# Kernel optimization log

Hardware: AMD Instinct MI355X
Metric: run time of the kernel (lower is better)

## Reference

```python
import jax, jax.numpy as jnp
import numpy as np

D_MODEL = 1024
N_HEADS = 16
HEAD_DIM = 64
BATCH = 4
SEQ = 2048


def setup_inputs() -> dict:
    key = jax.random.key(0)
    ks = jax.random.split(key, 5)
    scale = 1.0 / np.sqrt(D_MODEL)
    return {
        "x": jax.random.normal(ks[0], (BATCH, SEQ, D_MODEL), dtype=jnp.float32),
        "Wq": jax.random.normal(ks[1], (D_MODEL, N_HEADS * HEAD_DIM), dtype=jnp.float32) * scale,
        "Wk": jax.random.normal(ks[2], (D_MODEL, N_HEADS * HEAD_DIM), dtype=jnp.float32) * scale,
        "Wv": jax.random.normal(ks[3], (D_MODEL, N_HEADS * HEAD_DIM), dtype=jnp.float32) * scale,
        "Wo": jax.random.normal(ks[4], (N_HEADS * HEAD_DIM, D_MODEL), dtype=jnp.float32) * scale,
        "bo": jnp.zeros((D_MODEL,), dtype=jnp.float32),
    }


def reference(x, Wq, Wk, Wv, Wo, bo):
    B, S, _ = x.shape
    H, Dh = N_HEADS, HEAD_DIM
    # projections -> [B, H, S, Dh]
    q = (x @ Wq).reshape(B, S, H, Dh).transpose(0, 2, 1, 3)
    k = (x @ Wk).reshape(B, S, H, Dh).transpose(0, 2, 1, 3)
    v = (x @ Wv).reshape(B, S, H, Dh).transpose(0, 2, 1, 3)
    score = jnp.einsum("bhsd,bhtd->bhst", q, k) / jnp.sqrt(jnp.float32(Dh))
    causal = jnp.triu(jnp.ones((S, S), dtype=bool), k=1)
    score = jnp.where(causal, -jnp.inf, score)
    attn_probs = jax.nn.softmax(score, axis=-1)
    # dropout is identity in eval mode
    attn = jnp.einsum("bhst,bhtd->bhsd", attn_probs, v)
    out = attn.transpose(0, 2, 1, 3).reshape(B, S, H * Dh)
    out = out @ Wo + bo
    return (out, attn_probs)
```

## Files before the change

kernel.cpp:

```cpp
#include <hip/hip_runtime.h>
#include <hip/hip_bf16.h>

typedef __attribute__((ext_vector_type(8))) short bf16x8;
typedef __attribute__((ext_vector_type(4))) float f32x4;
typedef unsigned short ushort_t;

#define AS1 __attribute__((address_space(1)))
#define AS3 __attribute__((address_space(3)))

__device__ __forceinline__ void gload_lds16(const void* g, void* l) {
    __builtin_amdgcn_global_load_lds((const AS1 void*)g, (AS3 void*)l, 16, 0, 0);
}

__device__ __forceinline__ ushort_t f2b(float f) {
    unsigned u = __builtin_bit_cast(unsigned, f);
    unsigned r = (u + 0x7FFFu + ((u >> 16) & 1u)) >> 16;
    return (ushort_t)r;
}

__device__ __forceinline__ float b2f(short s) {
    unsigned v = ((unsigned)(ushort_t)s) << 16;
    return __builtin_bit_cast(float, v);
}

__global__ __launch_bounds__(256) void convert_x_kernel(const float* __restrict__ in,
                                                        ushort_t* __restrict__ out, int n4) {
    int i = blockIdx.x * blockDim.x + threadIdx.x;
    if (i < n4) {
        float4 f = ((const float4*)in)[i];
        ushort4 u;
        u.x = f2b(f.x); u.y = f2b(f.y); u.z = f2b(f.z); u.w = f2b(f.w);
        ((ushort4*)out)[i] = u;
    }
}

__global__ __launch_bounds__(256) void transpose_w_kernel(const float* __restrict__ W,
                                                          ushort_t* __restrict__ WT) {
    __shared__ float t[32][33];
    int n0 = blockIdx.x * 32, k0 = blockIdx.y * 32;
    int tx = threadIdx.x, ty = threadIdx.y;
    for (int i = 0; i < 4; ++i)
        t[ty + i * 8][tx] = W[(size_t)(k0 + ty + i * 8) * 1024 + n0 + tx];
    __syncthreads();
    for (int i = 0; i < 4; ++i)
        WT[(size_t)(n0 + ty + i * 8) * 1024 + k0 + tx] = f2b(t[tx][ty + i * 8]);
}

template <int N, int OUT_BF16>
__global__ __launch_bounds__(256) void gemm_kernel(const ushort_t* __restrict__ A,
                                                   const ushort_t* __restrict__ BT,
                                                   ushort_t* __restrict__ Cb,
                                                   float* __restrict__ Cf,
                                                   const float* __restrict__ bias) {
    const int K = 1024;
    __shared__ ushort_t As[2 * 128 * 32];
    __shared__ ushort_t Bs[2 * 128 * 32];
    int tid = threadIdx.x;
    int wid = tid >> 6, lane = tid & 63;
    int g = lane >> 4, lr = lane & 15;
    int m0 = blockIdx.x * 128, n0 = blockIdx.y * 128;
    int wm = wid >> 1, wn = wid & 1;

    f32x4 acc[4][4] = {};

    int c0 = wid * 2;
    int lrow = lane >> 2;
    int lcol = ((lane & 3) ^ ((lane >> 3) & 3)) * 8;
    const ushort_t* Ag0 = A  + (size_t)(m0 + c0 * 16 + lrow) * K + lcol;
    const ushort_t* Ag1 = A  + (size_t)(m0 + c0 * 16 + 16 + lrow) * K + lcol;
    const ushort_t* Bg0 = BT + (size_t)(n0 + c0 * 16 + lrow) * K + lcol;
    const ushort_t* Bg1 = BT + (size_t)(n0 + c0 * 16 + 16 + lrow) * K + lcol;

    int swzA = ((lr >> 1) & 3) << 4;

    auto stage = [&](int bufi, int kt) {
        char* a0 = (char*)As + bufi * 8192 + c0 * 1024;
        char* b0 = (char*)Bs + bufi * 8192 + c0 * 1024;
        gload_lds16(Ag0 + kt * 32, a0);
        gload_lds16(Ag1 + kt * 32, a0 + 1024);
        gload_lds16(Bg0 + kt * 32, b0);
        gload_lds16(Bg1 + kt * 32, b0 + 1024);
    };

    stage(0, 0);
    __syncthreads();
    int buf = 0;
    for (int kt = 0; kt < K / 32; ++kt) {
        if (kt + 1 < K / 32) stage(buf ^ 1, kt + 1);
        const char* ab = (const char*)As + buf * 8192;
        const char* bb = (const char*)Bs + buf * 8192;
        bf16x8 af[4], bfr[4];
#pragma unroll
        for (int m = 0; m < 4; ++m) {
            int row = wm * 64 + m * 16 + lr;
            af[m] = *(const bf16x8*)(ab + row * 64 + ((g * 16) ^ swzA));
        }
#pragma unroll
        for (int n = 0; n < 4; ++n) {
            int row = wn * 64 + n * 16 + lr;
            bfr[n] = *(const bf16x8*)(bb + row * 64 + ((g * 16) ^ swzA));
        }
#pragma unroll
        for (int m = 0; m < 4; ++m)
#pragma unroll
            for (int n = 0; n < 4; ++n)
                acc[m][n] = __builtin_amdgcn_mfma_f32_16x16x32_bf16(af[m], bfr[n], acc[m][n], 0, 0, 0);
        __syncthreads();
        buf ^= 1;
    }

#pragma unroll
    for (int m = 0; m < 4; ++m)
#pragma unroll
        for (int n = 0; n < 4; ++n) {
            int row0 = m0 + wm * 64 + m * 16 + g * 4;
            int col  = n0 + wn * 64 + n * 16 + lr;
#pragma unroll
            for (int r = 0; r < 4; ++r) {
                float v = acc[m][n][r];
                if (OUT_BF16)
                    Cb[(size_t)(row0 + r) * N + col] = f2b(v);
                else
                    Cf[(size_t)(row0 + r) * N + col] = v + bias[col];
            }
        }
}

__global__ __launch_bounds__(256) void vt_kernel(const ushort_t* __restrict__ Cqkv,
                                                 ushort_t* __restrict__ Vt) {
    int b = blockIdx.z, h = blockIdx.y, st = blockIdx.x;
    __shared__ ushort_t t[64][72];
    const ushort_t* src = Cqkv + (size_t)b * 2048 * 3072 + 2048 + (size_t)h * 64;
    int tid = threadIdx.x;
#pragma unroll
    for (int i = 0; i < 2; ++i) {
        int c = tid + i * 256;
        int sl = c >> 3, dc = (c & 7) * 8;
        *(bf16x8*)&t[sl][dc] = *(const bf16x8*)(src + (size_t)(st * 64 + sl) * 3072 + dc);
    }
    __syncthreads();
#pragma unroll
    for (int i = 0; i < 2; ++i) {
        int c = tid + i * 256;
        int d = c >> 3, sc = (c & 7) * 8;
        bf16x8 v;
#pragma unroll
        for (int j = 0; j < 8; ++j) v[j] = (short)t[sc + j][d];
        *(bf16x8*)(Vt + ((size_t)(b * 16 + h) * 64 + d) * 2048 + st * 64 + sc) = v;
    }
}

__global__ __launch_bounds__(256) void attn_kernel(const ushort_t* __restrict__ Cqkv,
                                                   const ushort_t* __restrict__ Vtg,
                                                   float* __restrict__ Pout,
                                                   ushort_t* __restrict__ Oout) {
    const int S = 2048, DQ = 3072;
    const float C1 = 0.18033688f;
    const float C2 = 5.77078016f;

    int z = (int)blockIdx.x + 32 * (int)blockIdx.y + 512 * (int)blockIdx.z;
    int h = (z >> 5) & 15, b = z >> 9;
    int qt = ((z & 31) + 13 * ((z >> 8) & 7)) & 31;
    int q0 = qt * 64;

    int tid = threadIdx.x, wid = tid >> 6, lane = tid & 63;
    int g = lane >> 4, lr = lane & 15;

    __shared__ ushort_t Ks[2][4096];
    __shared__ ushort_t Vs[2][4096];
    __shared__ ushort_t Pb[4096];
    char* PbB = (char*)Pb;

    const ushort_t* Qb = Cqkv + (size_t)b * S * DQ + (size_t)h * 64;
    const ushort_t* Kb = Cqkv + (size_t)b * S * DQ + 1024 + (size_t)h * 64;
    const ushort_t* Vb = Vtg + (size_t)((b * 16 + h) * 64) * 2048;
    float* Pbase = Pout + (((size_t)(b * 16 + h)) * S + q0) * S;

    int srow = lane >> 3;
    int scol = ((lane & 7) ^ (lane >> 3)) * 8;

    auto stageK = [&](int bufi, int tt) {
        char* dst = (char*)&Ks[bufi][0] + wid * 1024;
        gload_lds16(Kb + (size_t)(tt * 64 + wid * 8 + srow) * DQ + scol, dst);
        gload_lds16(Kb + (size_t)(tt * 64 + 32 + wid * 8 + srow) * DQ + scol, dst + 4096);
    };
    auto stageV = [&](int bufi, int tt) {
        char* dst = (char*)&Vs[bufi][0] + wid * 1024;
        gload_lds16(Vb + (size_t)(wid * 8 + srow) * 2048 + tt * 64 + scol, dst);
        gload_lds16(Vb + (size_t)(32 + wid * 8 + srow) * 2048 + tt * 64 + scol, dst + 4096);
    };

    bf16x8 qf[2];
    {
        const ushort_t* qp = Qb + (size_t)(q0 + wid * 16 + lr) * DQ + g * 8;
        qf[0] = *(const bf16x8*)qp;
        qf[1] = *(const bf16x8*)(qp + 32);
    }
    int qlg = wid * 16 + g * 4;

    float psum[4] = {0.f, 0.f, 0.f, 0.f};
    stageK(0, 0);
    __syncthreads();
    int buf = 0;
    for (int tt = 0; tt <= qt; ++tt) {
        if (tt < qt) stageK(buf ^ 1, tt + 1);
        const char* ksb = (const char*)&Ks[buf][0];
#pragma unroll
        for (int nb = 0; nb < 4; ++nb) {
            int row = nb * 16 + lr;
            int x = (row & 7) << 4;
            f32x4 s = {};
            s = __builtin_amdgcn_mfma_f32_16x16x32_bf16(qf[0], *(const bf16x8*)(ksb + row * 128 + ((g * 16) ^ x)), s, 0, 0, 0);
            s = __builtin_amdgcn_mfma_f32_16x16x32_bf16(qf[1], *(const bf16x8*)(ksb + row * 128 + ((64 + g * 16) ^ x)), s, 0, 0, 0);
            if (tt == qt) {
#pragma unroll
                for (int r = 0; r < 4; ++r)
                    if (row <= qlg + r) psum[r] += exp2f(fmaf(s[r], C1, -C2));
            } else {
#pragma unroll
                for (int r = 0; r < 4; ++r) psum[r] += exp2f(fmaf(s[r], C1, -C2));
            }
        }
        __syncthreads();
        buf ^= 1;
    }
    float lnl2[4];
#pragma unroll
    for (int r = 0; r < 4; ++r) {
        float v = psum[r];
        v += __shfl_xor(v, 1); v += __shfl_xor(v, 2);
        v += __shfl_xor(v, 4); v += __shfl_xor(v, 8);
        lnl2[r] = __log2f(v) + C2;
    }

    f32x4 Oacc[4] = {};
    stageK(buf, 0);
    stageV(buf, 0);
    __syncthreads();
    for (int tt = 0; tt <= qt; ++tt) {
        if (tt < qt) { stageK(buf ^ 1, tt + 1); stageV(buf ^ 1, tt + 1); }
        const char* ksb = (const char*)&Ks[buf][0];
        const char* vsb = (const char*)&Vs[buf][0];
#pragma unroll
        for (int nb = 0; nb < 4; ++nb) {
            int row = nb * 16 + lr;
            int x = (row & 7) << 4;
            f32x4 s = {};
            s = __builtin_amdgcn_mfma_f32_16x16x32_bf16(qf[0], *(const bf16x8*)(ksb + row * 128 + ((g * 16) ^ x)), s, 0, 0, 0);
            s = __builtin_amdgcn_mfma_f32_16x16x32_bf16(qf[1], *(const bf16x8*)(ksb + row * 128 + ((64 + g * 16) ^ x)), s, 0, 0, 0);
#pragma unroll
            for (int r = 0; r < 4; ++r) {
                float p = exp2f(fmaf(s[r], C1, -lnl2[r]));
                if (tt == qt && (row > qlg + r)) p = 0.f;
                int prow = qlg + r;
                *(ushort_t*)(PbB + ((prow * 128 + row * 2) ^ ((prow & 7) << 4))) = f2b(p);
            }
        }
        __builtin_amdgcn_wave_barrier();
#pragma unroll
        for (int kc = 0; kc < 2; ++kc) {
            int prow = wid * 16 + lr;
            bf16x8 pf = *(const bf16x8*)(PbB + ((prow * 128 + kc * 64 + g * 16) ^ ((prow & 7) << 4)));
#pragma unroll
            for (int nb = 0; nb < 4; ++nb) {
                int vrow = nb * 16 + lr;
                bf16x8 vf = *(const bf16x8*)(vsb + vrow * 128 + ((kc * 64 + g * 16) ^ ((vrow & 7) << 4)));
                Oacc[nb] = __builtin_amdgcn_mfma_f32_16x16x32_bf16(pf, vf, Oacc[nb], 0, 0, 0);
            }
        }
        {
            int row = wid * 16 + (lane >> 2);
            int c0 = (lane & 3) * 16;
            int x = (row & 7) << 4;
            bf16x8 p0 = *(const bf16x8*)(PbB + ((row * 128 + c0 * 2) ^ x));
            bf16x8 p1 = *(const bf16x8*)(PbB + ((row * 128 + c0 * 2 + 16) ^ x));
            float* dst = Pbase + (size_t)row * S + tt * 64 + c0;
            float4 w;
            w.x = b2f(p0[0]); w.y = b2f(p0[1]); w.z = b2f(p0[2]); w.w = b2f(p0[3]); ((float4*)dst)[0] = w;
            w.x = b2f(p0[4]); w.y = b2f(p0[5]); w.z = b2f(p0[6]); w.w = b2f(p0[7]); ((float4*)dst)[1] = w;
            w.x = b2f(p1[0]); w.y = b2f(p1[1]); w.z = b2f(p1[2]); w.w = b2f(p1[3]); ((float4*)dst)[2] = w;
            w.x = b2f(p1[4]); w.y = b2f(p1[5]); w.z = b2f(p1[6]); w.w = b2f(p1[7]); ((float4*)dst)[3] = w;
        }
        __syncthreads();
        buf ^= 1;
    }

    {
        int vsr = tid >> 2, vsc = (tid & 3) * 16;
        float4 zf = {0.f, 0.f, 0.f, 0.f};
        for (int tt = qt + 1; tt < 32; ++tt) {
            float* dst = Pbase + (size_t)vsr * S + tt * 64 + vsc;
#pragma unroll
            for (int j = 0; j < 4; ++j) ((float4*)dst)[j] = zf;
        }
    }

#pragma unroll
    for (int nb = 0; nb < 4; ++nb)
#pragma unroll
        for (int r = 0; r < 4; ++r) {
            int q = q0 + qlg + r;
            Oout[((size_t)b * S + q) * 1024 + h * 64 + nb * 16 + lr] = f2b(Oacc[nb][r]);
        }
}

extern "C" void kernel_launch(void* const* d_in, const int* in_sizes, int n_in,
                              void* d_out, int out_size, void* d_ws, size_t ws_size,
                              hipStream_t stream) {
    const float* x  = (const float*)d_in[0];
    const float* Wq = (const float*)d_in[1];
    const float* Wk = (const float*)d_in[2];
    const float* Wv = (const float*)d_in[3];
    const float* Wo = (const float*)d_in[4];
    const float* bo = (const float*)d_in[5];

    float* out  = (float*)d_out;
    float* Pout = out + (size_t)8388608;

    char* ws = (char*)d_ws;
    ushort_t* xb    = (ushort_t*)(ws);
    ushort_t* wqkv  = (ushort_t*)(ws + (16u << 20));
    ushort_t* wob   = (ushort_t*)(ws + (22u << 20));
    ushort_t* Cqkv  = (ushort_t*)(ws + (24u << 20));
    ushort_t* Vtw   = (ushort_t*)(ws + (72u << 20));
    ushort_t* attnb = (ushort_t*)(ws + (104u << 20));

    convert_x_kernel<<<8192, 256, 0, stream>>>(x, xb, 2097152);
    transpose_w_kernel<<<dim3(32, 32), dim3(32, 8), 0, stream>>>(Wq, wqkv);
    transpose_w_kernel<<<dim3(32, 32), dim3(32, 8), 0, stream>>>(Wk, wqkv + 1024 * 1024);
    transpose_w_kernel<<<dim3(32, 32), dim3(32, 8), 0, stream>>>(Wv, wqkv + 2 * 1024 * 1024);
    transpose_w_kernel<<<dim3(32, 32), dim3(32, 8), 0, stream>>>(Wo, wob);

    gemm_kernel<3072, 1><<<dim3(64, 24), 256, 0, stream>>>(xb, wqkv, Cqkv, nullptr, nullptr);

    vt_kernel<<<dim3(32, 16, 4), 256, 0, stream>>>(Cqkv, Vtw);

    attn_kernel<<<dim3(32, 16, 4), 256, 0, stream>>>(Cqkv, Vtw, Pout, attnb);

    gemm_kernel<1024, 0><<<dim3(64, 8), 256, 0, stream>>>(attnb, wob, nullptr, out, bo);
}
```

Baseline: 556.3 us.

## Transpose score MFMA so each lane owns a query row and stores P directly

The Q·K MFMA operands are swapped, so each lane holds four consecutive key scores for a single query row. This lets the probability tile go straight from registers to global memory as fp32 float4 stores, removing the staging through shared memory as bf16 and the read-back. The row-sum reduction becomes two cross-group shuffles instead of four. The bf16 copy for P·V is packed with v_cvt_pk_bf16_f32 into a per-wave LDS slice. The end-of-iteration __syncthreads is replaced by a vmcnt(4) wait plus s_barrier, so the P stores can stay in flight while the next tiles land; this relies on exact counting of outstanding memory ops.

```diff
diff --git a/kernel.cpp b/kernel.cpp
--- a/kernel.cpp
+++ b/kernel.cpp
@@ -4,6 +4,7 @@
 typedef __attribute__((ext_vector_type(8))) short bf16x8;
 typedef __attribute__((ext_vector_type(4))) float f32x4;
 typedef unsigned short ushort_t;
+typedef unsigned int uint_t;
 
 #define AS1 __attribute__((address_space(1)))
 #define AS3 __attribute__((address_space(3)))
@@ -16,11 +17,6 @@
     unsigned u = __builtin_bit_cast(unsigned, f);
     unsigned r = (u + 0x7FFFu + ((u >> 16) & 1u)) >> 16;
     return (ushort_t)r;
-}
-
-__device__ __forceinline__ float b2f(short s) {
-    unsigned v = ((unsigned)(ushort_t)s) << 16;
-    return __builtin_bit_cast(float, v);
 }
 
 __global__ __launch_bounds__(256) void convert_x_kernel(const float* __restrict__ in,
@@ -168,8 +164,8 @@
 
     __shared__ ushort_t Ks[2][4096];
     __shared__ ushort_t Vs[2][4096];
-    __shared__ ushort_t Pb[4096];
-    char* PbB = (char*)Pb;
+    __shared__ ushort_t Pl[4096];
+    char* PlB = (char*)Pl + wid * 2048;
 
     const ushort_t* Qb = Cqkv + (size_t)b * S * DQ + (size_t)h * 64;
     const ushort_t* Kb = Cqkv + (size_t)b * S * DQ + 1024 + (size_t)h * 64;
@@ -177,7 +173,7 @@
     float* Pbase = Pout + (((size_t)(b * 16 + h)) * S + q0) * S;
 
     int srow = lane >> 3;
-    int scol = ((lane & 7) ^ (lane >> 3)) * 8;
+    int scol = ((lane & 7) ^ srow) * 8;
 
     auto stageK = [&](int bufi, int tt) {
         char* dst = (char*)&Ks[bufi][0] + wid * 1024;
@@ -196,9 +192,9 @@
         qf[0] = *(const bf16x8*)qp;
         qf[1] = *(const bf16x8*)(qp + 32);
     }
-    int qlg = wid * 16 + g * 4;
-
-    float psum[4] = {0.f, 0.f, 0.f, 0.f};
+    int qloc = wid * 16 + lr;
+
+    float psum = 0.f;
     stageK(0, 0);
     __syncthreads();
     int buf = 0;
@@ -210,28 +206,23 @@
             int row = nb * 16 + lr;
             int x = (row & 7) << 4;
             f32x4 s = {};
-            s = __builtin_amdgcn_mfma_f32_16x16x32_bf16(qf[0], *(const bf16x8*)(ksb + row * 128 + ((g * 16) ^ x)), s, 0, 0, 0);
-            s = __builtin_amdgcn_mfma_f32_16x16x32_bf16(qf[1], *(const bf16x8*)(ksb + row * 128 + ((64 + g * 16) ^ x)), s, 0, 0, 0);
+            s = __builtin_amdgcn_mfma_f32_16x16x32_bf16(*(const bf16x8*)(ksb + row * 128 + ((g * 16) ^ x)), qf[0], s, 0, 0, 0);
+            s = __builtin_amdgcn_mfma_f32_16x16x32_bf16(*(const bf16x8*)(ksb + row * 128 + ((64 + g * 16) ^ x)), qf[1], s, 0, 0, 0);
             if (tt == qt) {
 #pragma unroll
                 for (int r = 0; r < 4; ++r)
-                    if (row <= qlg + r) psum[r] += exp2f(fmaf(s[r], C1, -C2));
+                    if (nb * 16 + g * 4 + r <= qloc) psum += exp2f(fmaf(s[r], C1, -C2));
             } else {
 #pragma unroll
-                for (int r = 0; r < 4; ++r) psum[r] += exp2f(fmaf(s[r], C1, -C2));
+                for (int r = 0; r < 4; ++r) psum += exp2f(fmaf(s[r], C1, -C2));
             }
         }
         __syncthreads();
         buf ^= 1;
     }
-    float lnl2[4];
-#pragma unroll
-    for (int r = 0; r < 4; ++r) {
-        float v = psum[r];
-        v += __shfl_xor(v, 1); v += __shfl_xor(v, 2);
-        v += __shfl_xor(v, 4); v += __shfl_xor(v, 8);
-        lnl2[r] = __log2f(v) + C2;
-    }
+    psum += __shfl_xor(psum, 16);
+    psum += __shfl_xor(psum, 32);
+    float lnl2 = __log2f(psum) + C2;
 
     f32x4 Oacc[4] = {};
     stageK(buf, 0);
@@ -241,26 +232,36 @@
         if (tt < qt) { stageK(buf ^ 1, tt + 1); stageV(buf ^ 1, tt + 1); }
         const char* ksb = (const char*)&Ks[buf][0];
         const char* vsb = (const char*)&Vs[buf][0];
+        f32x4 p[4];
 #pragma unroll
         for (int nb = 0; nb < 4; ++nb) {
             int row = nb * 16 + lr;
             int x = (row & 7) << 4;
             f32x4 s = {};
-            s = __builtin_amdgcn_mfma_f32_16x16x32_bf16(qf[0], *(const bf16x8*)(ksb + row * 128 + ((g * 16) ^ x)), s, 0, 0, 0);
-            s = __builtin_amdgcn_mfma_f32_16x16x32_bf16(qf[1], *(const bf16x8*)(ksb + row * 128 + ((64 + g * 16) ^ x)), s, 0, 0, 0);
+            s = __builtin_amdgcn_mfma_f32_16x16x32_bf16(*(const bf16x8*)(ksb + row * 128 + ((g * 16) ^ x)), qf[0], s, 0, 0, 0);
+            s = __builtin_amdgcn_mfma_f32_16x16x32_bf16(*(const bf16x8*)(ksb + row * 128 + ((64 + g * 16) ^ x)), qf[1], s, 0, 0, 0);
 #pragma unroll
             for (int r = 0; r < 4; ++r) {
-                float p = exp2f(fmaf(s[r], C1, -lnl2[r]));
-                if (tt == qt && (row > qlg + r)) p = 0.f;
-                int prow = qlg + r;
-                *(ushort_t*)(PbB + ((prow * 128 + row * 2) ^ ((prow & 7) << 4))) = f2b(p);
+                float v = exp2f(fmaf(s[r], C1, -lnl2));
+                if (tt == qt && (nb * 16 + g * 4 + r > qloc)) v = 0.f;
+                p[nb][r] = v;
             }
         }
+#pragma unroll
+        for (int nb = 0; nb < 4; ++nb)
+            *(f32x4*)(Pbase + (size_t)qloc * S + tt * 64 + nb * 16 + g * 4) = p[nb];
+#pragma unroll
+        for (int nb = 0; nb < 4; ++nb) {
+            uint_t w0, w1;
+            asm("v_cvt_pk_bf16_f32 %0, %1, %2" : "=v"(w0) : "v"(p[nb][0]), "v"(p[nb][1]));
+            asm("v_cvt_pk_bf16_f32 %0, %1, %2" : "=v"(w1) : "v"(p[nb][2]), "v"(p[nb][3]));
+            uint2 w; w.x = w0; w.y = w1;
+            *(uint2*)(PlB + ((lr * 128 + nb * 32 + g * 8) ^ ((lr & 7) << 4))) = w;
+        }
         __builtin_amdgcn_wave_barrier();
 #pragma unroll
         for (int kc = 0; kc < 2; ++kc) {
-            int prow = wid * 16 + lr;
-            bf16x8 pf = *(const bf16x8*)(PbB + ((prow * 128 + kc * 64 + g * 16) ^ ((prow & 7) << 4)));
+            bf16x8 pf = *(const bf16x8*)(PlB + ((lr * 128 + kc * 64 + g * 16) ^ ((lr & 7) << 4)));
 #pragma unroll
             for (int nb = 0; nb < 4; ++nb) {
                 int vrow = nb * 16 + lr;
@@ -268,20 +269,9 @@
                 Oacc[nb] = __builtin_amdgcn_mfma_f32_16x16x32_bf16(pf, vf, Oacc[nb], 0, 0, 0);
             }
         }
-        {
-            int row = wid * 16 + (lane >> 2);
-            int c0 = (lane & 3) * 16;
-            int x = (row & 7) << 4;
-            bf16x8 p0 = *(const bf16x8*)(PbB + ((row * 128 + c0 * 2) ^ x));
-            bf16x8 p1 = *(const bf16x8*)(PbB + ((row * 128 + c0 * 2 + 16) ^ x));
-            float* dst = Pbase + (size_t)row * S + tt * 64 + c0;
-            float4 w;
-            w.x = b2f(p0[0]); w.y = b2f(p0[1]); w.z = b2f(p0[2]); w.w = b2f(p0[3]); ((float4*)dst)[0] = w;
-            w.x = b2f(p0[4]); w.y = b2f(p0[5]); w.z = b2f(p0[6]); w.w = b2f(p0[7]); ((float4*)dst)[1] = w;
-            w.x = b2f(p1[0]); w.y = b2f(p1[1]); w.z = b2f(p1[2]); w.w = b2f(p1[3]); ((float4*)dst)[2] = w;
-            w.x = b2f(p1[4]); w.y = b2f(p1[5]); w.z = b2f(p1[6]); w.w = b2f(p1[7]); ((float4*)dst)[3] = w;
-        }
-        __syncthreads();
+        asm volatile("s_waitcnt vmcnt(4)" ::: "memory");
+        __builtin_amdgcn_s_barrier();
+        __builtin_amdgcn_sched_barrier(0);
         buf ^= 1;
     }
 
@@ -299,7 +289,7 @@
     for (int nb = 0; nb < 4; ++nb)
 #pragma unroll
         for (int r = 0; r < 4; ++r) {
-            int q = q0 + qlg + r;
+            int q = q0 + wid * 16 + g * 4 + r;
             Oout[((size_t)b * S + q) * 1024 + h * 64 + nb * 16 + lr] = f2b(Oacc[nb][r]);
         }
 }
```

Measured after the change: 485.8 us. -12.7%, faster.
